# Performance work log

Measured on AMD Instinct MI355X. Metric: run time of the kernel, lower is better.

## Reference

```python
import jax, jax.numpy as jnp
import numpy as np


def _glorot(key, shape):
    lim = np.sqrt(6.0 / (shape[-2] + shape[-1])).astype(np.float32)
    return jax.random.uniform(key, shape, jnp.float32, -lim, lim)


def setup_inputs() -> dict:
    key = jax.random.key(0)
    B, F, K, L = 8192, 256, 32768, 4
    H = 2 * F          # CouplingLayer(feat_size, feat_size * 2) hidden width
    half = F // 2      # affine coupling transforms half the features
    ks = jax.random.split(key, 6)
    return {
        "inputs": jax.random.normal(ks[0], (B, F), jnp.float32),
        "W1": _glorot(ks[1], (L, half, H)),
        "b1": jnp.zeros((L, H), jnp.float32),
        "Ws": _glorot(ks[2], (L, H, half)),
        "bs": jnp.zeros((L, half), jnp.float32),
        "Wt": _glorot(ks[3], (L, H, half)),
        "bt": jnp.zeros((L, half), jnp.float32),
        "prior": _glorot(ks[4], (K, F)),  # VQ codebook, GlorotUniform init as in source
    }


def _forward_flow(x, W1, b1, Ws, bs, Wt, bt):
    """Stack of affine coupling layers; returns (y, log|det J|) per sample."""
    L = W1.shape[0]
    jac = jnp.zeros((x.shape[0],), x.dtype)
    for l in range(L):  # small fixed layer count
        xa, xb = jnp.split(x, 2, axis=1)                 # [B, F/2] each
        h = jax.nn.relu(xa @ W1[l] + b1[l])              # [B, 2F]
        s_raw = h @ Ws[l] + bs[l]                        # [B, F/2]
        s = s_raw if l == L - 1 else jnp.tanh(s_raw)     # last layer: tf.identity
        t = h @ Wt[l] + bt[l]
        yb = xb * jnp.exp(s) + t
        jac = jac + jnp.sum(s, axis=1)
        x = jnp.concatenate([yb, xa], axis=1)            # swap halves for mixing
    return x, jac


def reference(inputs, W1, b1, Ws, bs, Wt, bt, prior):
    sg = jax.lax.stop_gradient
    x, jac = _forward_flow(inputs, W1, b1, Ws, bs, Wt, bt)   # [B, F], [B]
    # pairwise squared distance to codebook: [B, K]
    na = jnp.sum(x * x, axis=1, keepdims=True)               # [B, 1]
    nb = jnp.sum(prior * prior, axis=1)[None, :]             # [1, K]
    d = jnp.maximum(na - 2.0 * (x @ prior.T) + nb, 0.0)      # [B, K]
    target_ind = jnp.argmin(d, axis=1)                       # [B]
    target = prior[target_ind]                               # gather, [B, F]
    loss_1 = jnp.mean(jnp.sum((x - sg(target)) ** 2, axis=1) / 2)
    loss_2 = jnp.mean(jnp.sum((sg(x) - target) ** 2, axis=1) / 2)
    loss = loss_1 + 0.25 * loss_2 - jnp.mean(jac)
    return x, loss
```

## Files before the change

### kernel.cpp

```cpp
#include <hip/hip_runtime.h>
#include <hip/hip_fp8.h>
#include <stdint.h>

#define NB     8192
#define NF     256
#define NHALF  128
#define NHID   512
#define NLAY   4
#define NK     32768

#define SX     (1.0f / 16.0f)
#define SP     (256.0f)

typedef __attribute__((ext_vector_type(8))) short bf16x8;
typedef __attribute__((ext_vector_type(4))) float f32x4;
typedef __attribute__((ext_vector_type(8))) int i32x8;

static __device__ __forceinline__ unsigned short f2bf(float f) {
  union { float f; unsigned int u; } v; v.f = f;
  return (unsigned short)((v.u + 0x7FFFu + ((v.u >> 16) & 1u)) >> 16);
}
static __device__ __forceinline__ float bf2f(unsigned short u) {
  union { unsigned int u; float f; } v; v.u = ((unsigned int)u) << 16; return v.f;
}
static __device__ __forceinline__ unsigned char f2fp8(float f) {
  __hip_fp8_e4m3 q(f);
  return (unsigned char)q.__x;
}
static __device__ __forceinline__ float fp82f(unsigned char b) {
  __hip_fp8_e4m3 q; q.__x = b; return (float)q;
}

static __device__ __forceinline__ void load_lds16(const void* g, void* l) {
  __builtin_amdgcn_global_load_lds(
      (const __attribute__((address_space(1))) unsigned int*)g,
      (__attribute__((address_space(3))) unsigned int*)l, 16, 0, 0);
}

static __device__ __forceinline__ unsigned long long packsi(float v, int idx) {
  unsigned int b = __float_as_uint(v);
  b = (b & 0x80000000u) ? ~b : (b | 0x80000000u);
  return ((unsigned long long)b << 32) | (unsigned int)(~(unsigned int)idx);
}

static __device__ __forceinline__ float fast_tanh(float x) {
  const float xc = fminf(fmaxf(x, -15.f), 15.f);
  const float e2 = __expf(2.f * xc);
  return 1.f - 2.f / (e2 + 1.f);
}

static __device__ __forceinline__ int swadr(int kseg, int nrows, int row, int kin) {
  return (kseg * nrows + row) * 64 + (((kin >> 3) ^ (row & 7)) * 8) + (kin & 7);
}

static __device__ __forceinline__ void stage_seg(
    int g, unsigned short* dst,
    const unsigned short* __restrict__ W1T,
    const unsigned short* __restrict__ W2I,
    int wave, int lane, int bxr, int hswap)
{
  const int l = g / 24, s = g % 24;
  const int nc = ((s / 3) + bxr) & 7;
  const int t = s % 3;
  if (t == 0) {
    const unsigned short* W1l = W1T + (size_t)l * (NHID * NHALF) + (size_t)nc * 64 * 128;
#pragma unroll
    for (int u = 0; u < 4; u++) {
      const int chb = (u * 4 + wave) * 64;
      const int ch = chb + lane;
      const int kseg = ch >> 9, cs = ch & 511;
      const int row = cs >> 3, cc = (cs & 7) ^ (row & 7);
      load_lds16(W1l + (size_t)row * 128 + kseg * 64 + cc * 8, dst + chb * 8);
    }
  } else {
    const int half = (t - 1) ^ hswap;
    const unsigned short* W2l = W2I + (size_t)l * (NF * NHID) + nc * 64 + half * 32;
#pragma unroll
    for (int u = 0; u < 4; u++) {
      const int chb = (u * 4 + wave) * 64;
      const int ch = chb + lane;
      const int row = ch >> 2;
      const int cc = (ch & 3) ^ ((row >> 1) & 3);
      load_lds16(W2l + (size_t)row * NHID + cc * 8, dst + chb * 8);
    }
  }
}

__global__ __launch_bounds__(256, 2)
void flow_all(const float* __restrict__ in,
              const unsigned short* __restrict__ W1T,
              const unsigned short* __restrict__ W2I,
              const float* __restrict__ b1A,
              const float* __restrict__ bsA,
              const float* __restrict__ btA,
              float* __restrict__ xout,
              unsigned char* __restrict__ xf8,
              float* __restrict__ jac)
{
  __shared__ __align__(16) unsigned short Xb[2][16 * 128];
  __shared__ __align__(16) unsigned short Hs[16 * 64];
  __shared__ __align__(16) unsigned short Bs[3][8192];
  __shared__ float b1s[NLAY * NHID];
  __shared__ float bss[NLAY * NHALF];
  __shared__ float bts[NLAY * NHALF];
  __shared__ float jlds[3][16];
  const int tid = threadIdx.x;
  const int lane = tid & 63, wave = tid >> 6;
  const int q = lane >> 4, c = lane & 15;
  const int m0 = blockIdx.x * 16;
  const int bxr = blockIdx.x & 7;
  const int hswap = (blockIdx.x >> 3) & 1;

  stage_seg(0, Bs[0], W1T, W2I, wave, lane, bxr, hswap);

#pragma unroll
  for (int v = 0; v < 4; v++) {
    const int t4 = tid + v * 256;
    const int row = t4 >> 6, f4 = t4 & 63;
    const float4 d = *(const float4*)(in + (size_t)(m0 + row) * NF + f4 * 4);
    unsigned short* dst = Xb[f4 >> 5];
    const int feat = (f4 & 31) * 4;
    const float vals[4] = {d.x, d.y, d.z, d.w};
#pragma unroll
    for (int u = 0; u < 4; u++) {
      const int fe = feat + u;
      dst[swadr(fe >> 6, 16, row, fe & 63)] = f2bf(vals[u]);
    }
  }

#pragma unroll
  for (int v = 0; v < 8; v++) b1s[tid + v * 256] = b1A[tid + v * 256];
#pragma unroll
  for (int v = 0; v < 2; v++) {
    bss[tid + v * 256] = bsA[tid + v * 256];
    bts[tid + v * 256] = btA[tid + v * 256];
  }

  stage_seg(1, Bs[1], W1T, W2I, wave, lane, bxr, hswap);

  float jr[4] = {0.f, 0.f, 0.f, 0.f};
  bf16x8 af1[4];
  const f32x4 z = {0.f, 0.f, 0.f, 0.f};
  f32x4 acc2[4];

  for (int gs = 0; gs < 96; gs++) {
    if (gs < 95)
      asm volatile("s_waitcnt vmcnt(4) lgkmcnt(0)\n\ts_barrier" ::: "memory");
    else
      asm volatile("s_waitcnt vmcnt(0) lgkmcnt(0)\n\ts_barrier" ::: "memory");

    if (gs + 2 < 96) stage_seg(gs + 2, Bs[(gs + 2) % 3], W1T, W2I, wave, lane, bxr, hswap);

    const int l = gs / 24, s = gs % 24, typ = s % 3;
    const int nc8 = ((s / 3) + bxr) & 7;
    const unsigned short* B = Bs[gs % 3];
    unsigned short* XA = Xb[l & 1];
    unsigned short* XB = Xb[1 - (l & 1)];

    if (typ == 0) {
      if (s == 0) {
#pragma unroll
        for (int kw = 0; kw < 4; kw++) {
          const int kch = kw * 4 + q;
          af1[kw] = *(const bf16x8*)(XA + ((kch >> 3) * 16 + c) * 64 +
                                     (((kch & 7) ^ (c & 7)) * 8));
        }
#pragma unroll
        for (int j = 0; j < 4; j++) acc2[j] = z;
      }
      f32x4 acc1 = z;
      const int rb = wave * 16 + c;
#pragma unroll
      for (int kw = 0; kw < 4; kw++) {
        const int kseg = kw >> 1, g = (kw & 1) * 4 + q;
        const bf16x8 bf = *(const bf16x8*)(B + (kseg * 64 + rb) * 64 + ((g ^ (rb & 7)) * 8));
        acc1 = __builtin_amdgcn_mfma_f32_16x16x32_bf16(af1[kw], bf, acc1, 0, 0, 0);
      }
      const int hc = wave * 16 + c;
      const float bb = b1s[l * NHID + nc8 * 64 + hc];
#pragma unroll
      for (int r = 0; r < 4; r++) {
        float v = acc1[r] + bb;
        v = v > 0.f ? v : 0.f;
        Hs[swadr(0, 16, 4 * q + r, hc)] = f2bf(v);
      }
    } else {
      const int half = (typ - 1) ^ hswap;
      const bf16x8 afh = *(const bf16x8*)(Hs + c * 64 + (((half * 4 + q) ^ (c & 7)) * 8));
#pragma unroll
      for (int j = 0; j < 4; j++) {
        const int rb = wave * 64 + 16 * j + c;
        const bf16x8 bf = *(const bf16x8*)(B + rb * 32 + ((q ^ ((rb >> 1) & 3)) * 8));
        acc2[j] = __builtin_amdgcn_mfma_f32_16x16x32_bf16(afh, bf, acc2[j], 0, 0, 0);
      }
    }

    if (s == 23) {
      const int parity = c & 1;
      const int lastl = (l == NLAY - 1);
      const float* bsl = bss + l * NHALF;
      const float* btl = bts + l * NHALF;
#pragma unroll
      for (int j = 0; j < 4; j++) {
        const int col = wave * 64 + 16 * j + c;
#pragma unroll
        for (int r = 0; r < 4; r++) {
          const float val = acc2[j][r];
          const float oth = __shfl_xor(val, 1);
          if (!parity) {
            const int feat = col >> 1;
            float sv = val + bsl[feat];
            if (!lastl) sv = fast_tanh(sv);
            const float t = oth + btl[feat];
            const int row = 4 * q + r;
            const int xaddr = swadr(feat >> 6, 16, row, feat & 63);
            const float xb = bf2f(XB[xaddr]);
            const float yb = xb * __expf(sv) + t;
            jr[r] += sv;
            XB[xaddr] = f2bf(yb);
            if (l >= 2) {
              const int k = lastl ? feat : (NHALF + feat);
              const size_t grow = (size_t)(m0 + row) * NF;
              xout[grow + k] = yb;
              xf8[(size_t)(m0 + row) * 256 + k] = f2fp8(yb * SX);
            }
          }
        }
      }
    }
  }

  float v0[4];
#pragma unroll
  for (int r = 0; r < 4; r++) {
    float v = jr[r];
    v += __shfl_xor(v, 1); v += __shfl_xor(v, 2);
    v += __shfl_xor(v, 4); v += __shfl_xor(v, 8);
    if (c == 0) {
      if (wave) jlds[wave - 1][4 * q + r] = v;
      else v0[r] = v;
    }
  }
  __syncthreads();
  if (wave == 0 && c == 0) {
#pragma unroll
    for (int r = 0; r < 4; r++) {
      const int row = 4 * q + r;
      jac[m0 + row] = v0[r] + jlds[0][row] + jlds[1][row] + jlds[2][row];
    }
  }
}

__global__ __launch_bounds__(256, 2)
void vq_argmax(const unsigned char* __restrict__ X8,
               const unsigned char* __restrict__ P8,
               const float* __restrict__ nbh,
               unsigned long long* __restrict__ gbest)
{
  __shared__ __align__(16) unsigned char Bs[2][64 * 256];
  const int tid = threadIdx.x;
  const int lane = tid & 63, wave = tid >> 6;
  const int y = blockIdx.x & 15;
  const int m0 = (blockIdx.x >> 4) * 256;
  const int q = lane >> 4, c = lane & 15;
  const int mw = m0 + wave * 64;
  const int one = 0x7F7F7F7F;

  i32x8 af[4][2];
#pragma unroll
  for (int i = 0; i < 4; i++) {
    const unsigned char* xr = X8 + (size_t)(mw + 16 * i + c) * 256 + q * 32;
#pragma unroll
    for (int h = 0; h < 2; h++) {
      const int4 lo = *(const int4*)(xr + h * 128);
      const int4 hi = *(const int4*)(xr + h * 128 + 16);
      af[i][h] = (i32x8){lo.x, lo.y, lo.z, lo.w, hi.x, hi.y, hi.z, hi.w};
    }
  }

  float bestv[16];
  int besti[16];
#pragma unroll
  for (int t = 0; t < 16; t++) { bestv[t] = -1e30f; besti[t] = 0; }

  {
    const int n0s = y * 2048;
#pragma unroll
    for (int u = 0; u < 4; u++) {
      const int chb = (u * 4 + wave) * 64;
      const int ch = chb + lane;
      const int row = ch >> 4, gslot = ch & 15;
      load_lds16(P8 + (size_t)(n0s + row) * 256 + (gslot ^ (row & 15)) * 16,
                 Bs[0] + chb * 16);
    }
  }

  for (int nt = 0; nt < 32; nt++) {
    const int n0 = y * 2048 + nt * 64;
    __syncthreads();

    float nbr[4];
#pragma unroll
    for (int j = 0; j < 4; j++) nbr[j] = nbh[n0 + 16 * j + c];

    if (nt + 1 < 32) {
      const int n0s = n0 + 64;
      unsigned char* dst = Bs[(nt + 1) & 1];
#pragma unroll
      for (int u = 0; u < 4; u++) {
        const int chb = (u * 4 + wave) * 64;
        const int ch = chb + lane;
        const int row = ch >> 4, gslot = ch & 15;
        load_lds16(P8 + (size_t)(n0s + row) * 256 + (gslot ^ (row & 15)) * 16,
                   dst + chb * 16);
      }
    }

    const unsigned char* Bt = Bs[nt & 1];
    f32x4 acc[4][4];
#pragma unroll
    for (int i = 0; i < 4; i++)
#pragma unroll
      for (int j = 0; j < 4; j++)
        acc[i][j] = (f32x4){-nbr[j], -nbr[j], -nbr[j], -nbr[j]};

#pragma unroll
    for (int j = 0; j < 4; j++) {
      const unsigned char* base = Bt + (16 * j + c) * 256;
#pragma unroll
      for (int h = 0; h < 2; h++) {
        const int4 b0 = *(const int4*)(base + ((8 * h + 2 * q)     ^ c) * 16);
        const int4 b1 = *(const int4*)(base + ((8 * h + 2 * q + 1) ^ c) * 16);
        const i32x8 bf = (i32x8){b0.x, b0.y, b0.z, b0.w, b1.x, b1.y, b1.z, b1.w};
#pragma unroll
        for (int i = 0; i < 4; i++)
          acc[i][j] = __builtin_amdgcn_mfma_scale_f32_16x16x128_f8f6f4(
              af[i][h], bf, acc[i][j], 0, 0, 0, one, 0, one);
      }
    }

#pragma unroll
    for (int j = 0; j < 4; j++) {
      const int col = n0 + 16 * j + c;
#pragma unroll
      for (int i = 0; i < 4; i++)
#pragma unroll
        for (int r = 0; r < 4; r++) {
          const float sc = acc[i][j][r];
          const int t = i * 4 + r;
          if (sc > bestv[t]) { bestv[t] = sc; besti[t] = col; }
        }
    }
  }

#pragma unroll
  for (int t = 0; t < 16; t++) {
    float lv = bestv[t]; int li = besti[t];
#pragma unroll
    for (int mk = 8; mk >= 1; mk >>= 1) {
      const float ov = __shfl_xor(lv, mk);
      const int oi = __shfl_xor(li, mk);
      if (ov > lv || (ov == lv && oi < li)) { lv = ov; li = oi; }
    }
    if (c == 0) {
      const int row = mw + 16 * (t >> 2) + q * 4 + (t & 3);
      atomicMax(&gbest[row], packsi(lv, li));
    }
  }
}

__global__ void prep_all(const float* __restrict__ W1,
                         const float* __restrict__ Ws,
                         const float* __restrict__ Wt,
                         const float* __restrict__ prior,
                         unsigned short* __restrict__ W1T,
                         unsigned short* __restrict__ W2I,
                         unsigned char* __restrict__ p8,
                         float* __restrict__ nbh,
                         unsigned long long* __restrict__ gbest,
                         float* __restrict__ accum)
{
  __shared__ float ts[64 * 65];
  const int bx = blockIdx.x;
  const int tid = threadIdx.x;
  if (bx < 2048) {
    const int k = bx * 16 + (tid >> 4);
    const int l16 = tid & 15;
    float s = 0.f;
#pragma unroll
    for (int v = 0; v < 4; v++) {
      const int off = (v * 16 + l16) * 4;
      const float4 d = *(const float4*)(prior + (size_t)k * NF + off);
      uchar4 o;
      o.x = f2fp8(d.x * SP); o.y = f2fp8(d.y * SP);
      o.z = f2fp8(d.z * SP); o.w = f2fp8(d.w * SP);
      *(uchar4*)(p8 + (size_t)k * 256 + off) = o;
      const float q0 = fp82f(o.x), q1 = fp82f(o.y), q2 = fp82f(o.z), q3 = fp82f(o.w);
      s += q0 * q0 + q1 * q1 + q2 * q2 + q3 * q3;
    }
#pragma unroll
    for (int mk = 8; mk >= 1; mk >>= 1) s += __shfl_xor(s, mk);
    if (l16 == 0) nbh[k] = 0.5f * s * (SX / SP);
  } else if (bx < 2112) {
    const int job = bx - 2048;
    const int l = job >> 4, t = job & 15;
    const int k0 = (t >> 3) * 64, n0 = (t & 7) * 64;
    const float* src = W1 + (size_t)l * NHALF * NHID;
#pragma unroll
    for (int v = 0; v < 16; v++) {
      const int e = tid + v * 256;
      const int kk = e >> 6, nn = e & 63;
      ts[kk * 65 + nn] = src[(size_t)(k0 + kk) * NHID + n0 + nn];
    }
    __syncthreads();
    unsigned short* dst = W1T + (size_t)l * NHID * NHALF;
#pragma unroll
    for (int v = 0; v < 16; v++) {
      const int e = tid + v * 256;
      const int nn = e >> 6, kk = e & 63;
      dst[(size_t)(n0 + nn) * NHALF + k0 + kk] = f2bf(ts[kk * 65 + nn]);
    }
  } else if (bx < 2240) {
    const int job = bx - 2112;
    const int l = job >> 5, rem = job & 31;
    const int b = rem >> 4;
    const int k0 = ((rem >> 1) & 7) * 64;
    const int f0 = (rem & 1) * 64;
    const float* src = (b ? Wt : Ws) + (size_t)l * NHID * NHALF;
#pragma unroll
    for (int v = 0; v < 16; v++) {
      const int e = tid + v * 256;
      const int kk = e >> 6, nn = e & 63;
      ts[kk * 65 + nn] = src[(size_t)(k0 + kk) * NHALF + f0 + nn];
    }
    __syncthreads();
#pragma unroll
    for (int v = 0; v < 16; v++) {
      const int e = tid + v * 256;
      const int nn = e >> 6, kk = e & 63;
      W2I[((size_t)l * NF + 2 * (f0 + nn) + b) * NHID + k0 + kk] = f2bf(ts[kk * 65 + nn]);
    }
  } else {
    const int idx = (bx - 2240) * 256 + tid;
    if (idx < NB) gbest[idx] = 0ull;
    if (idx < 4) accum[idx] = 0.f;
  }
}

__global__ void vq_finalize(const float* __restrict__ X,
                            const float* __restrict__ prior,
                            const unsigned long long* __restrict__ gbest,
                            const float* __restrict__ jac,
                            float* __restrict__ accum,
                            float* __restrict__ loss)
{
  const int wave = threadIdx.x >> 6, lane = threadIdx.x & 63;
  const int gw = blockIdx.x * 4 + wave;
  float accd = 0.f, accj = 0.f;
  for (int r = 0; r < 8; r++) {
    const int row = gw * 8 + r;
    const unsigned int idx = ~(unsigned int)(gbest[row]);
    const float* x = X + (size_t)row * NF;
    const float* p = prior + (size_t)idx * NF;
#pragma unroll
    for (int u = 0; u < 4; u++) {
      const int d = lane + u * 64;
      const float df = x[d] - p[d];
      accd += df * df;
    }
    if (lane == 0) accj += jac[row];
  }
#pragma unroll
  for (int mk = 32; mk >= 1; mk >>= 1) {
    accd += __shfl_xor(accd, mk);
    accj += __shfl_xor(accj, mk);
  }
  __shared__ float sd[4], sj[4];
  if (lane == 0) { sd[wave] = accd; sj[wave] = accj; }
  __syncthreads();
  if (threadIdx.x == 0) {
    atomicAdd(&accum[0], sd[0] + sd[1] + sd[2] + sd[3]);
    atomicAdd(&accum[1], sj[0] + sj[1] + sj[2] + sj[3]);
    __threadfence();
    const unsigned int t = atomicAdd((unsigned int*)&accum[2], 1u);
    if (t == 255u) {
      const float d = atomicAdd(&accum[0], 0.f);
      const float jv = atomicAdd(&accum[1], 0.f);
      loss[0] = 1.25f * (0.5f * d / (float)NB) - jv / (float)NB;
    }
  }
}

extern "C" void kernel_launch(void* const* d_in, const int* in_sizes, int n_in,
                              void* d_out, int out_size, void* d_ws, size_t ws_size,
                              hipStream_t stream)
{
  (void)in_sizes; (void)n_in; (void)out_size; (void)ws_size;
  const float* inputs = (const float*)d_in[0];
  const float* W1 = (const float*)d_in[1];
  const float* b1 = (const float*)d_in[2];
  const float* Ws = (const float*)d_in[3];
  const float* bs = (const float*)d_in[4];
  const float* Wt = (const float*)d_in[5];
  const float* bt = (const float*)d_in[6];
  const float* prior = (const float*)d_in[7];

  char* p = (char*)d_ws;
  auto alloc = [&](size_t bytes) { char* r = p; p += (bytes + 255) & ~(size_t)255; return r; };
  unsigned short* W1T  = (unsigned short*)alloc((size_t)NLAY * NHID * NHALF * 2);
  unsigned short* W2I  = (unsigned short*)alloc((size_t)NLAY * NF * NHID * 2);
  unsigned char* P8    = (unsigned char*)alloc((size_t)NK * 256);
  float* NBH           = (float*)alloc((size_t)NK * 4);
  unsigned char* XF8   = (unsigned char*)alloc((size_t)NB * 256);
  float* JAC           = (float*)alloc((size_t)NB * 4);
  unsigned long long* GBEST = (unsigned long long*)alloc((size_t)NB * 8);
  float* ACC           = (float*)alloc(256);

  float* xout = (float*)d_out;
  float* loss = xout + (size_t)NB * NF;

  prep_all<<<dim3(2272), 256, 0, stream>>>(
      W1, Ws, Wt, prior, W1T, W2I, P8, NBH, GBEST, ACC);

  flow_all<<<dim3(NB / 16), 256, 0, stream>>>(
      inputs, W1T, W2I, b1, bs, bt, xout, XF8, JAC);

  vq_argmax<<<dim3(32 * 16), 256, 0, stream>>>(XF8, P8, NBH, GBEST);
  vq_finalize<<<dim3(256), 256, 0, stream>>>(xout, prior, GBEST, JAC, ACC, loss);
}
```

Baseline: 259.4 us.

## Double flow kernel row tile to 32 with 8 waves and deepen weight pipeline

The flow kernel now handles 32 batch rows per block using 512 threads arranged as two row groups of four column waves. Each staged weight segment in LDS is therefore reused by twice as many rows, and global weight traffic per row is halved. The staging ring goes from 3 to 5 buffers with a prefetch distance of 4, and the vmcnt waits are adjusted to match. The cost is more LDS per block (about 96KB) and only 256 blocks for the grid, which may limit occupancy and CU coverage.

```diff
diff --git a/kernel.cpp b/kernel.cpp
--- a/kernel.cpp
+++ b/kernel.cpp
@@ -65,8 +65,8 @@
   if (t == 0) {
     const unsigned short* W1l = W1T + (size_t)l * (NHID * NHALF) + (size_t)nc * 64 * 128;
 #pragma unroll
-    for (int u = 0; u < 4; u++) {
-      const int chb = (u * 4 + wave) * 64;
+    for (int u = 0; u < 2; u++) {
+      const int chb = (u * 8 + wave) * 64;
       const int ch = chb + lane;
       const int kseg = ch >> 9, cs = ch & 511;
       const int row = cs >> 3, cc = (cs & 7) ^ (row & 7);
@@ -76,8 +76,8 @@
     const int half = (t - 1) ^ hswap;
     const unsigned short* W2l = W2I + (size_t)l * (NF * NHID) + nc * 64 + half * 32;
 #pragma unroll
-    for (int u = 0; u < 4; u++) {
-      const int chb = (u * 4 + wave) * 64;
+    for (int u = 0; u < 2; u++) {
+      const int chb = (u * 8 + wave) * 64;
       const int ch = chb + lane;
       const int row = ch >> 2;
       const int cc = (ch & 3) ^ ((row >> 1) & 3);
@@ -86,7 +86,7 @@
   }
 }
 
-__global__ __launch_bounds__(256, 2)
+__global__ __launch_bounds__(512, 2)
 void flow_all(const float* __restrict__ in,
               const unsigned short* __restrict__ W1T,
               const unsigned short* __restrict__ W2I,
@@ -97,17 +97,18 @@
               unsigned char* __restrict__ xf8,
               float* __restrict__ jac)
 {
-  __shared__ __align__(16) unsigned short Xb[2][16 * 128];
-  __shared__ __align__(16) unsigned short Hs[16 * 64];
-  __shared__ __align__(16) unsigned short Bs[3][8192];
+  __shared__ __align__(16) unsigned short Xb[2][32 * 128];
+  __shared__ __align__(16) unsigned short Hs[32 * 64];
+  __shared__ __align__(16) unsigned short Bs[5][8192];
   __shared__ float b1s[NLAY * NHID];
   __shared__ float bss[NLAY * NHALF];
   __shared__ float bts[NLAY * NHALF];
-  __shared__ float jlds[3][16];
+  __shared__ float jlds[4][32];
   const int tid = threadIdx.x;
   const int lane = tid & 63, wave = tid >> 6;
+  const int rg = wave >> 2, cg = wave & 3;
   const int q = lane >> 4, c = lane & 15;
-  const int m0 = blockIdx.x * 16;
+  const int m0 = blockIdx.x * 32;
   const int bxr = blockIdx.x & 7;
   const int hswap = (blockIdx.x >> 3) & 1;
 
@@ -115,7 +116,7 @@
 
 #pragma unroll
   for (int v = 0; v < 4; v++) {
-    const int t4 = tid + v * 256;
+    const int t4 = tid + v * 512;
     const int row = t4 >> 6, f4 = t4 & 63;
     const float4 d = *(const float4*)(in + (size_t)(m0 + row) * NF + f4 * 4);
     unsigned short* dst = Xb[f4 >> 5];
@@ -124,19 +125,18 @@
 #pragma unroll
     for (int u = 0; u < 4; u++) {
       const int fe = feat + u;
-      dst[swadr(fe >> 6, 16, row, fe & 63)] = f2bf(vals[u]);
-    }
-  }
-
-#pragma unroll
-  for (int v = 0; v < 8; v++) b1s[tid + v * 256] = b1A[tid + v * 256];
-#pragma unroll
-  for (int v = 0; v < 2; v++) {
-    bss[tid + v * 256] = bsA[tid + v * 256];
-    bts[tid + v * 256] = btA[tid + v * 256];
-  }
+      dst[swadr(fe >> 6, 32, row, fe & 63)] = f2bf(vals[u]);
+    }
+  }
+
+#pragma unroll
+  for (int v = 0; v < 4; v++) b1s[tid + v * 512] = b1A[tid + v * 512];
+  bss[tid] = bsA[tid];
+  bts[tid] = btA[tid];
 
   stage_seg(1, Bs[1], W1T, W2I, wave, lane, bxr, hswap);
+  stage_seg(2, Bs[2], W1T, W2I, wave, lane, bxr, hswap);
+  stage_seg(3, Bs[3], W1T, W2I, wave, lane, bxr, hswap);
 
   float jr[4] = {0.f, 0.f, 0.f, 0.f};
   bf16x8 af1[4];
@@ -144,16 +144,20 @@
   f32x4 acc2[4];
 
   for (int gs = 0; gs < 96; gs++) {
-    if (gs < 95)
+    if (gs < 93)
+      asm volatile("s_waitcnt vmcnt(6) lgkmcnt(0)\n\ts_barrier" ::: "memory");
+    else if (gs == 93)
       asm volatile("s_waitcnt vmcnt(4) lgkmcnt(0)\n\ts_barrier" ::: "memory");
+    else if (gs == 94)
+      asm volatile("s_waitcnt vmcnt(2) lgkmcnt(0)\n\ts_barrier" ::: "memory");
     else
       asm volatile("s_waitcnt vmcnt(0) lgkmcnt(0)\n\ts_barrier" ::: "memory");
 
-    if (gs + 2 < 96) stage_seg(gs + 2, Bs[(gs + 2) % 3], W1T, W2I, wave, lane, bxr, hswap);
+    if (gs + 4 < 96) stage_seg(gs + 4, Bs[(gs + 4) % 5], W1T, W2I, wave, lane, bxr, hswap);
 
     const int l = gs / 24, s = gs % 24, typ = s % 3;
     const int nc8 = ((s / 3) + bxr) & 7;
-    const unsigned short* B = Bs[gs % 3];
+    const unsigned short* B = Bs[gs % 5];
     unsigned short* XA = Xb[l & 1];
     unsigned short* XB = Xb[1 - (l & 1)];
 
@@ -162,34 +166,35 @@
 #pragma unroll
         for (int kw = 0; kw < 4; kw++) {
           const int kch = kw * 4 + q;
-          af1[kw] = *(const bf16x8*)(XA + ((kch >> 3) * 16 + c) * 64 +
+          af1[kw] = *(const bf16x8*)(XA + ((kch >> 3) * 32 + rg * 16 + c) * 64 +
                                      (((kch & 7) ^ (c & 7)) * 8));
         }
 #pragma unroll
         for (int j = 0; j < 4; j++) acc2[j] = z;
       }
       f32x4 acc1 = z;
-      const int rb = wave * 16 + c;
+      const int rb = cg * 16 + c;
 #pragma unroll
       for (int kw = 0; kw < 4; kw++) {
         const int kseg = kw >> 1, g = (kw & 1) * 4 + q;
         const bf16x8 bf = *(const bf16x8*)(B + (kseg * 64 + rb) * 64 + ((g ^ (rb & 7)) * 8));
         acc1 = __builtin_amdgcn_mfma_f32_16x16x32_bf16(af1[kw], bf, acc1, 0, 0, 0);
       }
-      const int hc = wave * 16 + c;
+      const int hc = cg * 16 + c;
       const float bb = b1s[l * NHID + nc8 * 64 + hc];
 #pragma unroll
       for (int r = 0; r < 4; r++) {
         float v = acc1[r] + bb;
         v = v > 0.f ? v : 0.f;
-        Hs[swadr(0, 16, 4 * q + r, hc)] = f2bf(v);
+        Hs[swadr(0, 32, rg * 16 + 4 * q + r, hc)] = f2bf(v);
       }
     } else {
       const int half = (typ - 1) ^ hswap;
-      const bf16x8 afh = *(const bf16x8*)(Hs + c * 64 + (((half * 4 + q) ^ (c & 7)) * 8));
+      const bf16x8 afh = *(const bf16x8*)(Hs + (rg * 16 + c) * 64 +
+                                          (((half * 4 + q) ^ (c & 7)) * 8));
 #pragma unroll
       for (int j = 0; j < 4; j++) {
-        const int rb = wave * 64 + 16 * j + c;
+        const int rb = cg * 64 + 16 * j + c;
         const bf16x8 bf = *(const bf16x8*)(B + rb * 32 + ((q ^ ((rb >> 1) & 3)) * 8));
         acc2[j] = __builtin_amdgcn_mfma_f32_16x16x32_bf16(afh, bf, acc2[j], 0, 0, 0);
       }
@@ -202,7 +207,7 @@
       const float* btl = bts + l * NHALF;
 #pragma unroll
       for (int j = 0; j < 4; j++) {
-        const int col = wave * 64 + 16 * j + c;
+        const int col = cg * 64 + 16 * j + c;
 #pragma unroll
         for (int r = 0; r < 4; r++) {
           const float val = acc2[j][r];
@@ -212,8 +217,8 @@
             float sv = val + bsl[feat];
             if (!lastl) sv = fast_tanh(sv);
             const float t = oth + btl[feat];
-            const int row = 4 * q + r;
-            const int xaddr = swadr(feat >> 6, 16, row, feat & 63);
+            const int row = rg * 16 + 4 * q + r;
+            const int xaddr = swadr(feat >> 6, 32, row, feat & 63);
             const float xb = bf2f(XB[xaddr]);
             const float yb = xb * __expf(sv) + t;
             jr[r] += sv;
@@ -230,25 +235,16 @@
     }
   }
 
-  float v0[4];
 #pragma unroll
   for (int r = 0; r < 4; r++) {
     float v = jr[r];
     v += __shfl_xor(v, 1); v += __shfl_xor(v, 2);
     v += __shfl_xor(v, 4); v += __shfl_xor(v, 8);
-    if (c == 0) {
-      if (wave) jlds[wave - 1][4 * q + r] = v;
-      else v0[r] = v;
-    }
+    if (c == 0) jlds[cg][rg * 16 + 4 * q + r] = v;
   }
   __syncthreads();
-  if (wave == 0 && c == 0) {
-#pragma unroll
-    for (int r = 0; r < 4; r++) {
-      const int row = 4 * q + r;
-      jac[m0 + row] = v0[r] + jlds[0][row] + jlds[1][row] + jlds[2][row];
-    }
-  }
+  if (tid < 32)
+    jac[m0 + tid] = jlds[0][tid] + jlds[1][tid] + jlds[2][tid] + jlds[3][tid];
 }
 
 __global__ __launch_bounds__(256, 2)
@@ -522,7 +518,7 @@
   prep_all<<<dim3(2272), 256, 0, stream>>>(
       W1, Ws, Wt, prior, W1T, W2I, P8, NBH, GBEST, ACC);
 
-  flow_all<<<dim3(NB / 16), 256, 0, stream>>>(
+  flow_all<<<dim3(NB / 32), 512, 0, stream>>>(
       inputs, W1T, W2I, b1, bs, bt, xout, XF8, JAC);
 
   vq_argmax<<<dim3(32 * 16), 256, 0, stream>>>(XF8, P8, NBH, GBEST);
```

Measured after the change: 257.0 us. No clear change (-0.9%).
